# Performance work log

Measured on AMD Instinct MI355X. Metric: run time of the kernel, lower is better.

## Reference

```python
import jax, jax.numpy as jnp
import numpy as np
from jax import lax

TAU = 0.25
N_TIMESTEPS = 12
OUTPUT_TICKS = 4
INPUT_DIM = 1024
HIDDEN = 1024
OUTPUT_DIM = 1024
CLEANUP = 512
BATCH = 1024
W_SD = 0.1


def setup_inputs() -> dict:
    key = jax.random.key(0)
    ks = jax.random.split(key, 6)
    inputs = jax.random.normal(ks[0], (BATCH, N_TIMESTEPS, INPUT_DIM), dtype=jnp.float32)
    w_oh = W_SD * jax.random.normal(ks[1], (INPUT_DIM, HIDDEN), dtype=jnp.float32)
    w_hp = W_SD * jax.random.normal(ks[2], (HIDDEN, OUTPUT_DIM), dtype=jnp.float32)
    w_pp = W_SD * jax.random.normal(ks[3], (OUTPUT_DIM, OUTPUT_DIM), dtype=jnp.float32)
    w_pc = W_SD * jax.random.normal(ks[4], (OUTPUT_DIM, CLEANUP), dtype=jnp.float32)
    w_cp = W_SD * jax.random.normal(ks[5], (CLEANUP, OUTPUT_DIM), dtype=jnp.float32)
    bias_h = jnp.zeros((HIDDEN,), jnp.float32)
    bias_p = jnp.zeros((OUTPUT_DIM,), jnp.float32)
    bias_c = jnp.zeros((CLEANUP,), jnp.float32)
    return {"inputs": inputs, "w_oh": w_oh, "w_hp": w_hp, "w_pp": w_pp,
            "w_pc": w_pc, "w_cp": w_cp, "bias_h": bias_h, "bias_p": bias_p,
            "bias_c": bias_c}


def reference(inputs, w_oh, w_hp, w_pp, w_pc, w_cp, bias_h, bias_p, bias_c):
    B = inputs.shape[0]
    act = jax.nn.sigmoid
    # time-major input stream: step t consumes o_input[:, t-1, :]
    x = jnp.swapaxes(inputs, 0, 1)  # [T, B, I]

    in_h0 = jnp.zeros((B, HIDDEN), jnp.float32)
    in_p0 = jnp.zeros((B, OUTPUT_DIM), jnp.float32)
    in_c0 = jnp.zeros((B, CLEANUP), jnp.float32)
    carry0 = (in_h0, in_p0, in_c0, in_h0 + 0.5, in_p0 + 0.5, in_c0 + 0.5)

    def step(carry, o_t):
        in_h, in_p, in_c, a_h, a_p, a_c = carry
        # leaky-integrator blends; hp/pp/cp/pc all use PREVIOUS step activations
        h = TAU * (o_t @ w_oh + bias_h) + (1.0 - TAU) * in_h
        p = TAU * (a_h @ w_hp + a_p @ w_pp + a_c @ w_cp + bias_p) + (1.0 - TAU) * in_p
        c = TAU * (a_p @ w_pc + bias_c) + (1.0 - TAU) * in_c
        a_p_new = act(p)
        new_carry = (h, p, c, act(h), a_p_new, act(c))
        return new_carry, a_p_new

    _, act_p_seq = lax.scan(step, carry0, x)  # [T, B, OUTPUT_DIM]
    return act_p_seq[-OUTPUT_TICKS:]  # [OUTPUT_TICKS, B, OUTPUT_DIM]
```

## Files before the change

kernel.cpp:

```cpp
#include <hip/hip_runtime.h>
#include <cstdint>
#include <cstddef>


typedef _Float16 half8 __attribute__((ext_vector_type(8)));
typedef float floatx4 __attribute__((ext_vector_type(4)));

__device__ __forceinline__ void async_cp16(const void* g, void* l) {
  __builtin_amdgcn_global_load_lds(
      (const __attribute__((address_space(1))) void*)g,
      (__attribute__((address_space(3))) void*)l, 16, 0, 0);
}

__device__ __forceinline__ float sigmoidf_(float x) {
  return 1.f / (1.f + __expf(-x));
}

__global__ __launch_bounds__(256) void k_transpose(
    const float* __restrict__ src, int K, int N,
    _Float16* __restrict__ dst, int dst_ld, int k_off) {
  __shared__ float tile[64][65];
  const int k0 = blockIdx.y * 64, n0 = blockIdx.x * 64;
  const int tx = threadIdx.x & 63, ty = threadIdx.x >> 6;
#pragma unroll
  for (int j = 0; j < 16; ++j) {
    int kr = j * 4 + ty;
    tile[kr][tx] = src[(size_t)(k0 + kr) * N + n0 + tx];
  }
  __syncthreads();
#pragma unroll
  for (int j = 0; j < 16; ++j) {
    int nr = j * 4 + ty;
    dst[(size_t)(n0 + nr) * dst_ld + k_off + k0 + tx] = (_Float16)tile[tx][nr];
  }
}

__global__ __launch_bounds__(256) void k_pack_frag(
    const float* __restrict__ src, int N, _Float16* __restrict__ dst,
    int kStride, int kOffChunks) {
  __shared__ float tile[64][65];
  const int k0 = blockIdx.y * 64, n0 = blockIdx.x * 64;
  const int tx = threadIdx.x & 63, ty = threadIdx.x >> 6;
#pragma unroll
  for (int jj = 0; jj < 16; ++jj) {
    int kr = jj * 4 + ty;
    tile[kr][tx] = src[(size_t)(k0 + kr) * N + n0 + tx];
  }
  __syncthreads();
  const int j = threadIdx.x >> 6, lane = threadIdx.x & 63;
  const int r16 = lane & 15, quad = lane >> 4;
#pragma unroll
  for (int c = 0; c < 2; ++c) {
    half8 v;
#pragma unroll
    for (int u = 0; u < 8; ++u)
      v[u] = (_Float16)tile[c * 32 + quad * 8 + u][j * 16 + r16];
    const int kcG = kOffChunks + blockIdx.y * 2 + c;
    *(half8*)(dst + ((size_t)(blockIdx.x * kStride + kcG) * 4 + j) * 512 +
              lane * 8) = v;
  }
}

__global__ __launch_bounds__(256) void k_prep(
    const float* __restrict__ x, _Float16* __restrict__ U,
    _Float16* __restrict__ AH0, _Float16* __restrict__ AP0,
    _Float16* __restrict__ AC0, float* __restrict__ Pst,
    float* __restrict__ Cst) {
  const int id = blockIdx.x * 256 + threadIdx.x;
  const int b = id >> 10, i = id & 1023;
  const float* xb = x + (size_t)b * 12 * 1024 + i;
  float g = 0.f;
#pragma unroll
  for (int t = 0; t < 11; ++t) {
    g = xb[t * 1024] + 0.75f * g;
    U[(size_t)t * 1048576 + id] = (_Float16)g;
  }
  AH0[id] = (_Float16)0.5f;
  AP0[id] = (_Float16)0.5f;
  Pst[id] = 0.f;
  if (i < 512) {
    AC0[b * 512 + i] = (_Float16)0.5f;
    Cst[b * 512 + i] = 0.f;
  }
}

__global__ __launch_bounds__(256, 3) void k_gemm_big(
    const _Float16* __restrict__ A, const _Float16* __restrict__ B,
    const float* __restrict__ bias, _Float16* __restrict__ dst, int mode) {
  __shared__ __align__(16) _Float16 sA[128 * 64];
  __shared__ __align__(16) _Float16 sB[128 * 64];
  const int tid = threadIdx.x;
  const int lane = tid & 63, w = tid >> 6;
  const int lin = blockIdx.x;
  const int chunk = gridDim.x >> 6;
  const int xcd = lin & 7;
  const int j0 = lin >> 3;
  const int bx = j0 & 7;
  const int by = xcd * chunk + (j0 >> 3);
  const int mBase = by * 128, nBase = bx * 128;
  const int r16 = lane & 15, quad = lane >> 4;
  const int lrow = lane >> 3;
  const int gsw = ((lane & 7) ^ lrow) * 8;
  const int wr = w >> 1, wc = w & 1;

  const floatx4 zero = {0.f, 0.f, 0.f, 0.f};
  floatx4 acc[4][4];
#pragma unroll
  for (int i = 0; i < 4; ++i)
#pragma unroll
    for (int j = 0; j < 4; ++j) acc[i][j] = zero;

  const _Float16* Abase = A + (size_t)(mBase + w * 32 + lrow) * 1024 + gsw;
  const _Float16* Bbase = B + (size_t)(nBase + w * 32 + lrow) * 1024 + gsw;
  _Float16* sAw = sA + (w * 32) * 64;
  _Float16* sBw = sB + (w * 32) * 64;
  const _Float16* sa = sA + (size_t)wr * 64 * 64;
  const _Float16* sb = sB + (size_t)wc * 64 * 64;

  for (int kt = 0; kt < 16; ++kt) {
    const int k0 = kt << 6;
#pragma unroll
    for (int q = 0; q < 4; ++q)
      async_cp16(Abase + (size_t)q * 8192 + k0, sAw + q * 512);
#pragma unroll
    for (int q = 0; q < 4; ++q)
      async_cp16(Bbase + (size_t)q * 8192 + k0, sBw + q * 512);
    asm volatile("s_waitcnt vmcnt(0)" ::: "memory");
    __syncthreads();
#pragma unroll
    for (int kk = 0; kk < 2; ++kk) {
      const int sw = ((kk * 4 + quad) ^ (r16 & 7)) * 8;
      half8 af[4], bf[4];
#pragma unroll
      for (int i = 0; i < 4; ++i)
        af[i] = *(const half8*)&sa[(i * 16 + r16) * 64 + sw];
#pragma unroll
      for (int j = 0; j < 4; ++j)
        bf[j] = *(const half8*)&sb[(j * 16 + r16) * 64 + sw];
#pragma unroll
      for (int i = 0; i < 4; ++i)
#pragma unroll
        for (int j = 0; j < 4; ++j)
          acc[i][j] = __builtin_amdgcn_mfma_f32_16x16x32_f16(af[i], bf[j],
                                                             acc[i][j], 0, 0, 0);
    }
    __syncthreads();
  }

  if (mode == 0) {
    const int tm1 = mBase >> 10;
    const float beta = 1.f - __powf(0.75f, (float)(tm1 + 1));
    _Float16* o = dst + (size_t)(mBase + 1024) * 1024;
#pragma unroll
    for (int i = 0; i < 4; ++i)
#pragma unroll
      for (int j = 0; j < 4; ++j) {
        const int n = nBase + wc * 64 + j * 16 + r16;
#pragma unroll
        for (int r = 0; r < 4; ++r) {
          const int row = wr * 64 + i * 16 + quad * 4 + r;
          const float h = 0.25f * acc[i][j][r] + beta * bias[n];
          o[(size_t)row * 1024 + n] = (_Float16)sigmoidf_(h);
        }
      }
  } else {
    _Float16* o = dst + (size_t)mBase * 1024;
#pragma unroll
    for (int i = 0; i < 4; ++i)
#pragma unroll
      for (int j = 0; j < 4; ++j) {
        const int n = nBase + wc * 64 + j * 16 + r16;
#pragma unroll
        for (int r = 0; r < 4; ++r) {
          const int row = wr * 64 + i * 16 + quad * 4 + r;
          o[(size_t)row * 1024 + n] = (_Float16)(0.25f * (acc[i][j][r] + bias[n]));
        }
      }
  }
}

__global__ __launch_bounds__(256, 3) void k_step(
    const _Float16* __restrict__ Qt, const _Float16* __restrict__ APc,
    const _Float16* __restrict__ ACc, _Float16* __restrict__ APn,
    _Float16* __restrict__ ACn, const _Float16* __restrict__ Wrf,
    const _Float16* __restrict__ Wcf, const float* __restrict__ bias_c,
    float* __restrict__ Pst, float* __restrict__ Cst,
    float* __restrict__ out_t) {
  __shared__ float red[4][2][4][4][64];
  const int lane = threadIdx.x & 63, w = threadIdx.x >> 6;
  const int r16 = lane & 15, quad = lane >> 4;
  const int blk = blockIdx.x;
  const bool isP = blk < 512;
  int mBase, nt;
  if (isP) {
    mBase = (blk >> 4) * 32;
    nt = blk & 15;
  } else {
    const int b = blk - 512;
    mBase = (b >> 3) * 32;
    nt = b & 7;
  }
  const int nBase = nt * 64;
  const floatx4 zero = {0.f, 0.f, 0.f, 0.f};
  floatx4 acc[2][4];
#pragma unroll
  for (int i = 0; i < 2; ++i)
#pragma unroll
    for (int j = 0; j < 4; ++j) acc[i][j] = zero;

  half8 abuf[4][2], bbuf[4][4];
  auto MM = [&](half8* af, half8* bf) {
#pragma unroll
    for (int i = 0; i < 2; ++i)
#pragma unroll
      for (int j = 0; j < 4; ++j)
        acc[i][j] = __builtin_amdgcn_mfma_f32_16x16x32_f16(af[i], bf[j],
                                                           acc[i][j], 0, 0, 0);
  };

  if (isP) {
    const int kcBase = w * 12;
    auto LDA = [&](int c) {
      const int kc = kcBase + c, kg = kc * 32;
      half8* af = abuf[c & 3];
      if (kc < 32) {
        af[0] = *(const half8*)(APc + (size_t)(mBase + r16) * 1024 + kg + quad * 8);
        af[1] = *(const half8*)(APc + (size_t)(mBase + 16 + r16) * 1024 + kg + quad * 8);
      } else {
        af[0] = *(const half8*)(ACc + (size_t)(mBase + r16) * 512 + (kg - 1024) + quad * 8);
        af[1] = *(const half8*)(ACc + (size_t)(mBase + 16 + r16) * 512 + (kg - 1024) + quad * 8);
      }
    };
    auto LDB = [&](int c) {
      const int kc = kcBase + c;
      const _Float16* wp = Wrf + (size_t)(nt * 48 + kc) * 2048 + lane * 8;
      half8* bf = bbuf[c & 3];
#pragma unroll
      for (int j = 0; j < 4; ++j) bf[j] = *(const half8*)(wp + j * 512);
    };
    LDA(0); LDA(1); LDA(2); LDA(3);
    LDB(0); LDB(1); LDB(2);
#pragma unroll
    for (int c = 0; c < 12; ++c) {
      if (c + 3 < 12) LDB(c + 3);
      MM(abuf[c & 3], bbuf[c & 3]);
      if (c + 4 < 12) LDA(c + 4);
    }
  } else {
    const int kcBase = w * 8;
    auto LDA = [&](int c) {
      const int kc = kcBase + c, kg = kc * 32;
      half8* af = abuf[c & 3];
      af[0] = *(const half8*)(APc + (size_t)(mBase + r16) * 1024 + kg + quad * 8);
      af[1] = *(const half8*)(APc + (size_t)(mBase + 16 + r16) * 1024 + kg + quad * 8);
    };
    auto LDB = [&](int c) {
      const int kc = kcBase + c;
      const _Float16* wp = Wcf + (size_t)(nt * 32 + kc) * 2048 + lane * 8;
      half8* bf = bbuf[c & 3];
#pragma unroll
      for (int j = 0; j < 4; ++j) bf[j] = *(const half8*)(wp + j * 512);
    };
    LDA(0); LDA(1); LDA(2); LDA(3);
    LDB(0); LDB(1); LDB(2);
#pragma unroll
    for (int c = 0; c < 8; ++c) {
      if (c + 3 < 8) LDB(c + 3);
      MM(abuf[c & 3], bbuf[c & 3]);
      if (c + 4 < 8) LDA(c + 4);
    }
  }

  const int n_ep = nBase + w * 16 + r16;
  _Float16 qv[2][4];
  float sv[2][4];
  float biasn = 0.f;
  if (isP) {
#pragma unroll
    for (int i = 0; i < 2; ++i)
#pragma unroll
      for (int r = 0; r < 4; ++r) {
        const size_t o = (size_t)(mBase + i * 16 + quad * 4 + r) * 1024 + n_ep;
        qv[i][r] = Qt[o];
        sv[i][r] = Pst[o];
      }
  } else {
    biasn = bias_c[n_ep];
#pragma unroll
    for (int i = 0; i < 2; ++i)
#pragma unroll
      for (int r = 0; r < 4; ++r) {
        const size_t o = (size_t)(mBase + i * 16 + quad * 4 + r) * 512 + n_ep;
        sv[i][r] = Cst[o];
      }
  }

#pragma unroll
  for (int i = 0; i < 2; ++i)
#pragma unroll
    for (int j = 0; j < 4; ++j)
#pragma unroll
      for (int r = 0; r < 4; ++r) red[w][i][j][r][lane] = acc[i][j][r];
  asm volatile("s_waitcnt lgkmcnt(0)" ::: "memory");
  __builtin_amdgcn_s_barrier();

  if (isP) {
#pragma unroll
    for (int i = 0; i < 2; ++i) {
#pragma unroll
      for (int r = 0; r < 4; ++r) {
        float v = 0.f;
#pragma unroll
        for (int q = 0; q < 4; ++q) v += red[q][i][w][r][lane];
        const int b = mBase + i * 16 + quad * 4 + r;
        const size_t o = (size_t)b * 1024 + n_ep;
        const float pn = 0.25f * v + (float)qv[i][r] + 0.75f * sv[i][r];
        Pst[o] = pn;
        const float a = sigmoidf_(pn);
        APn[o] = (_Float16)a;
        if (out_t) out_t[o] = a;
      }
    }
  } else {
#pragma unroll
    for (int i = 0; i < 2; ++i) {
#pragma unroll
      for (int r = 0; r < 4; ++r) {
        float v = 0.f;
#pragma unroll
        for (int q = 0; q < 4; ++q) v += red[q][i][w][r][lane];
        const int b = mBase + i * 16 + quad * 4 + r;
        const size_t o = (size_t)b * 512 + n_ep;
        const float cn = 0.25f * (v + biasn) + 0.75f * sv[i][r];
        Cst[o] = cn;
        ACn[o] = (_Float16)sigmoidf_(cn);
      }
    }
  }
}

extern "C" void kernel_launch(void* const* d_in, const int* in_sizes, int n_in,
                              void* d_out, int out_size, void* d_ws,
                              size_t ws_size, hipStream_t stream) {
  const float* x      = (const float*)d_in[0];
  const float* w_oh   = (const float*)d_in[1];
  const float* w_hp   = (const float*)d_in[2];
  const float* w_pp   = (const float*)d_in[3];
  const float* w_pc   = (const float*)d_in[4];
  const float* w_cp   = (const float*)d_in[5];
  const float* bias_h = (const float*)d_in[6];
  const float* bias_p = (const float*)d_in[7];
  const float* bias_c = (const float*)d_in[8];
  float* out = (float*)d_out;

  uint8_t* p = (uint8_t*)d_ws;
  _Float16* Wrf  = (_Float16*)p; p += (size_t)1024 * 1536 * 2;
  _Float16* Wcf  = (_Float16*)p; p += (size_t)512 * 1024 * 2;
  _Float16* WohT = (_Float16*)p; p += (size_t)1024 * 1024 * 2;
  _Float16* Whp  = (_Float16*)p; p += (size_t)1024 * 1024 * 2;
  _Float16* U    = (_Float16*)p; p += (size_t)11 * 1048576 * 2;
  _Float16* AH   = (_Float16*)p; p += (size_t)12 * 1048576 * 2;
  _Float16* Q    = (_Float16*)p; p += (size_t)12 * 1048576 * 2;
  _Float16* AP0  = (_Float16*)p; p += (size_t)1048576 * 2;
  _Float16* AP1  = (_Float16*)p; p += (size_t)1048576 * 2;
  _Float16* AC0  = (_Float16*)p; p += (size_t)512 * 1024 * 2;
  _Float16* AC1  = (_Float16*)p; p += (size_t)512 * 1024 * 2;
  float* Pst = (float*)p; p += (size_t)1048576 * 4;
  float* Cst = (float*)p; p += (size_t)512 * 1024 * 4;

  const dim3 blk256(256);
  k_transpose<<<dim3(16, 16), blk256, 0, stream>>>(w_oh, 1024, 1024, WohT, 1024, 0);
  k_transpose<<<dim3(16, 16), blk256, 0, stream>>>(w_hp, 1024, 1024, Whp, 1024, 0);
  k_pack_frag<<<dim3(16, 16), blk256, 0, stream>>>(w_pp, 1024, Wrf, 48, 0);
  k_pack_frag<<<dim3(16, 8),  blk256, 0, stream>>>(w_cp, 1024, Wrf, 48, 32);
  k_pack_frag<<<dim3(8, 16),  blk256, 0, stream>>>(w_pc, 512, Wcf, 32, 0);
  k_prep<<<4096, blk256, 0, stream>>>(x, U, AH, AP0, AC0, Pst, Cst);
  k_gemm_big<<<dim3(8 * 88), blk256, 0, stream>>>(U, WohT, bias_h, AH, 0);
  k_gemm_big<<<dim3(8 * 96), blk256, 0, stream>>>(AH, Whp, bias_p, Q, 1);
  for (int t = 0; t < 12; ++t) {
    const _Float16* APc = (t & 1) ? AP1 : AP0;
    _Float16* APn       = (t & 1) ? AP0 : AP1;
    const _Float16* ACc = (t & 1) ? AC1 : AC0;
    _Float16* ACn       = (t & 1) ? AC0 : AC1;
    float* ot = (t >= 8) ? out + (size_t)(t - 8) * 1048576 : (float*)nullptr;
    k_step<<<dim3(768), blk256, 0, stream>>>(Q + (size_t)t * 1048576, APc,
                                             ACc, APn, ACn, Wrf, Wcf, bias_c,
                                             Pst, Cst, ot);
  }
}
```

Before: 385.2 us.

## Halve step-kernel N tile to double block count and merge weight-prep kernels

The recurrent step kernel now gives each block a 32x32 output tile instead of 32x64. This doubles the grid to 1536 blocks and raises the occupancy hint from 3 to 6 blocks per CU, with fewer accumulators and a shallower 3-stage load pipeline. The five weight transpose/pack kernels are merged into one launch to cut launch overhead. In exchange, activation rows are re-read by twice as many blocks and there is less prefetch depth per block.

```diff
diff --git a/kernel.cpp b/kernel.cpp
--- a/kernel.cpp
+++ b/kernel.cpp
@@ -16,11 +16,10 @@
   return 1.f / (1.f + __expf(-x));
 }
 
-__global__ __launch_bounds__(256) void k_transpose(
-    const float* __restrict__ src, int K, int N,
-    _Float16* __restrict__ dst, int dst_ld, int k_off) {
-  __shared__ float tile[64][65];
-  const int k0 = blockIdx.y * 64, n0 = blockIdx.x * 64;
+__device__ __forceinline__ void transpose_dev(
+    const float* __restrict__ src, int N, _Float16* __restrict__ dst,
+    int dst_ld, int k_off, int bx, int by, float (*tile)[65]) {
+  const int k0 = by * 64, n0 = bx * 64;
   const int tx = threadIdx.x & 63, ty = threadIdx.x >> 6;
 #pragma unroll
   for (int j = 0; j < 16; ++j) {
@@ -35,11 +34,10 @@
   }
 }
 
-__global__ __launch_bounds__(256) void k_pack_frag(
+__device__ __forceinline__ void pack_dev(
     const float* __restrict__ src, int N, _Float16* __restrict__ dst,
-    int kStride, int kOffChunks) {
-  __shared__ float tile[64][65];
-  const int k0 = blockIdx.y * 64, n0 = blockIdx.x * 64;
+    int kStride, int kOffChunks, int bx, int by, float (*tile)[65]) {
+  const int k0 = by * 64, n0 = bx * 64;
   const int tx = threadIdx.x & 63, ty = threadIdx.x >> 6;
 #pragma unroll
   for (int jj = 0; jj < 16; ++jj) {
@@ -55,9 +53,33 @@
 #pragma unroll
     for (int u = 0; u < 8; ++u)
       v[u] = (_Float16)tile[c * 32 + quad * 8 + u][j * 16 + r16];
-    const int kcG = kOffChunks + blockIdx.y * 2 + c;
-    *(half8*)(dst + ((size_t)(blockIdx.x * kStride + kcG) * 4 + j) * 512 +
-              lane * 8) = v;
+    const int kcG = kOffChunks + by * 2 + c;
+    *(half8*)(dst + ((size_t)(bx * kStride + kcG) * 4 + j) * 512 + lane * 8) = v;
+  }
+}
+
+__global__ __launch_bounds__(256) void k_wprep(
+    const float* __restrict__ w_oh, const float* __restrict__ w_hp,
+    const float* __restrict__ w_pp, const float* __restrict__ w_cp,
+    const float* __restrict__ w_pc, _Float16* __restrict__ WohT,
+    _Float16* __restrict__ Whp, _Float16* __restrict__ Wrf,
+    _Float16* __restrict__ Wcf) {
+  __shared__ float tile[64][65];
+  const int blk = blockIdx.x;
+  if (blk < 256) {
+    transpose_dev(w_oh, 1024, WohT, 1024, 0, blk & 15, blk >> 4, tile);
+  } else if (blk < 512) {
+    const int t = blk - 256;
+    transpose_dev(w_hp, 1024, Whp, 1024, 0, t & 15, t >> 4, tile);
+  } else if (blk < 768) {
+    const int t = blk - 512;
+    pack_dev(w_pp, 1024, Wrf, 48, 0, t & 15, t >> 4, tile);
+  } else if (blk < 896) {
+    const int t = blk - 768;
+    pack_dev(w_cp, 1024, Wrf, 48, 32, t & 15, t >> 4, tile);
+  } else {
+    const int t = blk - 896;
+    pack_dev(w_pc, 512, Wcf, 32, 0, t & 7, t >> 3, tile);
   }
 }
 
@@ -179,41 +201,42 @@
   }
 }
 
-__global__ __launch_bounds__(256, 3) void k_step(
+__global__ __launch_bounds__(256, 6) void k_step(
     const _Float16* __restrict__ Qt, const _Float16* __restrict__ APc,
     const _Float16* __restrict__ ACc, _Float16* __restrict__ APn,
     _Float16* __restrict__ ACn, const _Float16* __restrict__ Wrf,
     const _Float16* __restrict__ Wcf, const float* __restrict__ bias_c,
     float* __restrict__ Pst, float* __restrict__ Cst,
     float* __restrict__ out_t) {
-  __shared__ float red[4][2][4][4][64];
+  __shared__ float red[4][2][2][4][64];
   const int lane = threadIdx.x & 63, w = threadIdx.x >> 6;
   const int r16 = lane & 15, quad = lane >> 4;
   const int blk = blockIdx.x;
-  const bool isP = blk < 512;
-  int mBase, nt;
+  const bool isP = blk < 1024;
+  int mBase, nBase, ntG, jhalf;
   if (isP) {
-    mBase = (blk >> 4) * 32;
-    nt = blk & 15;
-  } else {
-    const int b = blk - 512;
-    mBase = (b >> 3) * 32;
-    nt = b & 7;
-  }
-  const int nBase = nt * 64;
+    mBase = (blk >> 5) * 32;
+    const int nt = blk & 31;
+    nBase = nt * 32; ntG = nt >> 1; jhalf = nt & 1;
+  } else {
+    const int b = blk - 1024;
+    mBase = (b >> 4) * 32;
+    const int nt = b & 15;
+    nBase = nt * 32; ntG = nt >> 1; jhalf = nt & 1;
+  }
   const floatx4 zero = {0.f, 0.f, 0.f, 0.f};
-  floatx4 acc[2][4];
+  floatx4 acc[2][2];
 #pragma unroll
   for (int i = 0; i < 2; ++i)
 #pragma unroll
-    for (int j = 0; j < 4; ++j) acc[i][j] = zero;
-
-  half8 abuf[4][2], bbuf[4][4];
+    for (int j = 0; j < 2; ++j) acc[i][j] = zero;
+
+  half8 abuf[3][2], bbuf[3][2];
   auto MM = [&](half8* af, half8* bf) {
 #pragma unroll
     for (int i = 0; i < 2; ++i)
 #pragma unroll
-      for (int j = 0; j < 4; ++j)
+      for (int j = 0; j < 2; ++j)
         acc[i][j] = __builtin_amdgcn_mfma_f32_16x16x32_f16(af[i], bf[j],
                                                            acc[i][j], 0, 0, 0);
   };
@@ -222,7 +245,7 @@
     const int kcBase = w * 12;
     auto LDA = [&](int c) {
       const int kc = kcBase + c, kg = kc * 32;
-      half8* af = abuf[c & 3];
+      half8* af = abuf[c % 3];
       if (kc < 32) {
         af[0] = *(const half8*)(APc + (size_t)(mBase + r16) * 1024 + kg + quad * 8);
         af[1] = *(const half8*)(APc + (size_t)(mBase + 16 + r16) * 1024 + kg + quad * 8);
@@ -233,72 +256,69 @@
     };
     auto LDB = [&](int c) {
       const int kc = kcBase + c;
-      const _Float16* wp = Wrf + (size_t)(nt * 48 + kc) * 2048 + lane * 8;
-      half8* bf = bbuf[c & 3];
-#pragma unroll
-      for (int j = 0; j < 4; ++j) bf[j] = *(const half8*)(wp + j * 512);
+      const _Float16* wp =
+          Wrf + ((size_t)(ntG * 48 + kc) * 4 + jhalf * 2) * 512 + lane * 8;
+      half8* bf = bbuf[c % 3];
+      bf[0] = *(const half8*)(wp);
+      bf[1] = *(const half8*)(wp + 512);
     };
-    LDA(0); LDA(1); LDA(2); LDA(3);
+    LDA(0); LDA(1); LDA(2);
     LDB(0); LDB(1); LDB(2);
 #pragma unroll
     for (int c = 0; c < 12; ++c) {
-      if (c + 3 < 12) LDB(c + 3);
-      MM(abuf[c & 3], bbuf[c & 3]);
-      if (c + 4 < 12) LDA(c + 4);
+      MM(abuf[c % 3], bbuf[c % 3]);
+      if (c + 3 < 12) { LDB(c + 3); LDA(c + 3); }
     }
   } else {
     const int kcBase = w * 8;
     auto LDA = [&](int c) {
       const int kc = kcBase + c, kg = kc * 32;
-      half8* af = abuf[c & 3];
+      half8* af = abuf[c % 3];
       af[0] = *(const half8*)(APc + (size_t)(mBase + r16) * 1024 + kg + quad * 8);
       af[1] = *(const half8*)(APc + (size_t)(mBase + 16 + r16) * 1024 + kg + quad * 8);
     };
     auto LDB = [&](int c) {
       const int kc = kcBase + c;
-      const _Float16* wp = Wcf + (size_t)(nt * 32 + kc) * 2048 + lane * 8;
-      half8* bf = bbuf[c & 3];
-#pragma unroll
-      for (int j = 0; j < 4; ++j) bf[j] = *(const half8*)(wp + j * 512);
+      const _Float16* wp =
+          Wcf + ((size_t)(ntG * 32 + kc) * 4 + jhalf * 2) * 512 + lane * 8;
+      half8* bf = bbuf[c % 3];
+      bf[0] = *(const half8*)(wp);
+      bf[1] = *(const half8*)(wp + 512);
     };
-    LDA(0); LDA(1); LDA(2); LDA(3);
+    LDA(0); LDA(1); LDA(2);
     LDB(0); LDB(1); LDB(2);
 #pragma unroll
     for (int c = 0; c < 8; ++c) {
-      if (c + 3 < 8) LDB(c + 3);
-      MM(abuf[c & 3], bbuf[c & 3]);
-      if (c + 4 < 8) LDA(c + 4);
-    }
-  }
-
-  const int n_ep = nBase + w * 16 + r16;
-  _Float16 qv[2][4];
-  float sv[2][4];
+      MM(abuf[c % 3], bbuf[c % 3]);
+      if (c + 3 < 8) { LDB(c + 3); LDA(c + 3); }
+    }
+  }
+
+  const int i_ep = w >> 1, j_ep = w & 1;
+  const int n_ep = nBase + j_ep * 16 + r16;
+  _Float16 qv[4];
+  float sv[4];
   float biasn = 0.f;
   if (isP) {
 #pragma unroll
-    for (int i = 0; i < 2; ++i)
-#pragma unroll
-      for (int r = 0; r < 4; ++r) {
-        const size_t o = (size_t)(mBase + i * 16 + quad * 4 + r) * 1024 + n_ep;
-        qv[i][r] = Qt[o];
-        sv[i][r] = Pst[o];
-      }
+    for (int r = 0; r < 4; ++r) {
+      const size_t o = (size_t)(mBase + i_ep * 16 + quad * 4 + r) * 1024 + n_ep;
+      qv[r] = Qt[o];
+      sv[r] = Pst[o];
+    }
   } else {
     biasn = bias_c[n_ep];
 #pragma unroll
-    for (int i = 0; i < 2; ++i)
-#pragma unroll
-      for (int r = 0; r < 4; ++r) {
-        const size_t o = (size_t)(mBase + i * 16 + quad * 4 + r) * 512 + n_ep;
-        sv[i][r] = Cst[o];
-      }
+    for (int r = 0; r < 4; ++r) {
+      const size_t o = (size_t)(mBase + i_ep * 16 + quad * 4 + r) * 512 + n_ep;
+      sv[r] = Cst[o];
+    }
   }
 
 #pragma unroll
   for (int i = 0; i < 2; ++i)
 #pragma unroll
-    for (int j = 0; j < 4; ++j)
+    for (int j = 0; j < 2; ++j)
 #pragma unroll
       for (int r = 0; r < 4; ++r) red[w][i][j][r][lane] = acc[i][j][r];
   asm volatile("s_waitcnt lgkmcnt(0)" ::: "memory");
@@ -306,35 +326,29 @@
 
   if (isP) {
 #pragma unroll
-    for (int i = 0; i < 2; ++i) {
-#pragma unroll
-      for (int r = 0; r < 4; ++r) {
-        float v = 0.f;
-#pragma unroll
-        for (int q = 0; q < 4; ++q) v += red[q][i][w][r][lane];
-        const int b = mBase + i * 16 + quad * 4 + r;
-        const size_t o = (size_t)b * 1024 + n_ep;
-        const float pn = 0.25f * v + (float)qv[i][r] + 0.75f * sv[i][r];
-        Pst[o] = pn;
-        const float a = sigmoidf_(pn);
-        APn[o] = (_Float16)a;
-        if (out_t) out_t[o] = a;
-      }
-    }
-  } else {
-#pragma unroll
-    for (int i = 0; i < 2; ++i) {
-#pragma unroll
-      for (int r = 0; r < 4; ++r) {
-        float v = 0.f;
-#pragma unroll
-        for (int q = 0; q < 4; ++q) v += red[q][i][w][r][lane];
-        const int b = mBase + i * 16 + quad * 4 + r;
-        const size_t o = (size_t)b * 512 + n_ep;
-        const float cn = 0.25f * (v + biasn) + 0.75f * sv[i][r];
-        Cst[o] = cn;
-        ACn[o] = (_Float16)sigmoidf_(cn);
-      }
+    for (int r = 0; r < 4; ++r) {
+      float v = 0.f;
+#pragma unroll
+      for (int q = 0; q < 4; ++q) v += red[q][i_ep][j_ep][r][lane];
+      const int b = mBase + i_ep * 16 + quad * 4 + r;
+      const size_t o = (size_t)b * 1024 + n_ep;
+      const float pn = 0.25f * v + (float)qv[r] + 0.75f * sv[r];
+      Pst[o] = pn;
+      const float a = sigmoidf_(pn);
+      APn[o] = (_Float16)a;
+      if (out_t) out_t[o] = a;
+    }
+  } else {
+#pragma unroll
+    for (int r = 0; r < 4; ++r) {
+      float v = 0.f;
+#pragma unroll
+      for (int q = 0; q < 4; ++q) v += red[q][i_ep][j_ep][r][lane];
+      const int b = mBase + i_ep * 16 + quad * 4 + r;
+      const size_t o = (size_t)b * 512 + n_ep;
+      const float cn = 0.25f * (v + biasn) + 0.75f * sv[r];
+      Cst[o] = cn;
+      ACn[o] = (_Float16)sigmoidf_(cn);
     }
   }
 }
@@ -369,11 +383,8 @@
   float* Cst = (float*)p; p += (size_t)512 * 1024 * 4;
 
   const dim3 blk256(256);
-  k_transpose<<<dim3(16, 16), blk256, 0, stream>>>(w_oh, 1024, 1024, WohT, 1024, 0);
-  k_transpose<<<dim3(16, 16), blk256, 0, stream>>>(w_hp, 1024, 1024, Whp, 1024, 0);
-  k_pack_frag<<<dim3(16, 16), blk256, 0, stream>>>(w_pp, 1024, Wrf, 48, 0);
-  k_pack_frag<<<dim3(16, 8),  blk256, 0, stream>>>(w_cp, 1024, Wrf, 48, 32);
-  k_pack_frag<<<dim3(8, 16),  blk256, 0, stream>>>(w_pc, 512, Wcf, 32, 0);
+  k_wprep<<<dim3(1024), blk256, 0, stream>>>(w_oh, w_hp, w_pp, w_cp, w_pc,
+                                             WohT, Whp, Wrf, Wcf);
   k_prep<<<4096, blk256, 0, stream>>>(x, U, AH, AP0, AC0, Pst, Cst);
   k_gemm_big<<<dim3(8 * 88), blk256, 0, stream>>>(U, WohT, bias_h, AH, 0);
   k_gemm_big<<<dim3(8 * 96), blk256, 0, stream>>>(AH, Whp, bias_p, Q, 1);
@@ -383,8 +394,8 @@
     const _Float16* ACc = (t & 1) ? AC1 : AC0;
     _Float16* ACn       = (t & 1) ? AC0 : AC1;
     float* ot = (t >= 8) ? out + (size_t)(t - 8) * 1048576 : (float*)nullptr;
-    k_step<<<dim3(768), blk256, 0, stream>>>(Q + (size_t)t * 1048576, APc,
-                                             ACc, APn, ACn, Wrf, Wcf, bias_c,
-                                             Pst, Cst, ot);
-  }
-}
+    k_step<<<dim3(1536), blk256, 0, stream>>>(Q + (size_t)t * 1048576, APc,
+                                              ACc, APn, ACn, Wrf, Wcf, bias_c,
+                                              Pst, Cst, ot);
+  }
+}
```

New measurement: 491.2 us. +27.5%, slower.

## Merge weight-prep kernels and shrink big GEMM N-tile to 64 for occupancy

Applied to the files above, without the earlier changes.

Folds the five weight transpose/pack launches into a single k_wprep kernel that dispatches on block index, removing four launches. It also halves the N tile of the big GEMMs from 128 to 64, doubling the grid and raising the launch-bounds occupancy hint from 3 to 5. The smaller tile gives more blocks to spread across CUs, but each A tile is now fetched for twice as many blocks and there is less MFMA work per LDS load.

```diff
diff --git a/kernel.cpp b/kernel.cpp
--- a/kernel.cpp
+++ b/kernel.cpp
@@ -16,11 +16,10 @@
   return 1.f / (1.f + __expf(-x));
 }
 
-__global__ __launch_bounds__(256) void k_transpose(
-    const float* __restrict__ src, int K, int N,
-    _Float16* __restrict__ dst, int dst_ld, int k_off) {
-  __shared__ float tile[64][65];
-  const int k0 = blockIdx.y * 64, n0 = blockIdx.x * 64;
+__device__ __forceinline__ void transpose_dev(
+    const float* __restrict__ src, int N, _Float16* __restrict__ dst,
+    int dst_ld, int k_off, int bx, int by, float (*tile)[65]) {
+  const int k0 = by * 64, n0 = bx * 64;
   const int tx = threadIdx.x & 63, ty = threadIdx.x >> 6;
 #pragma unroll
   for (int j = 0; j < 16; ++j) {
@@ -35,11 +34,10 @@
   }
 }
 
-__global__ __launch_bounds__(256) void k_pack_frag(
+__device__ __forceinline__ void pack_dev(
     const float* __restrict__ src, int N, _Float16* __restrict__ dst,
-    int kStride, int kOffChunks) {
-  __shared__ float tile[64][65];
-  const int k0 = blockIdx.y * 64, n0 = blockIdx.x * 64;
+    int kStride, int kOffChunks, int bx, int by, float (*tile)[65]) {
+  const int k0 = by * 64, n0 = bx * 64;
   const int tx = threadIdx.x & 63, ty = threadIdx.x >> 6;
 #pragma unroll
   for (int jj = 0; jj < 16; ++jj) {
@@ -55,9 +53,33 @@
 #pragma unroll
     for (int u = 0; u < 8; ++u)
       v[u] = (_Float16)tile[c * 32 + quad * 8 + u][j * 16 + r16];
-    const int kcG = kOffChunks + blockIdx.y * 2 + c;
-    *(half8*)(dst + ((size_t)(blockIdx.x * kStride + kcG) * 4 + j) * 512 +
-              lane * 8) = v;
+    const int kcG = kOffChunks + by * 2 + c;
+    *(half8*)(dst + ((size_t)(bx * kStride + kcG) * 4 + j) * 512 + lane * 8) = v;
+  }
+}
+
+__global__ __launch_bounds__(256) void k_wprep(
+    const float* __restrict__ w_oh, const float* __restrict__ w_hp,
+    const float* __restrict__ w_pp, const float* __restrict__ w_cp,
+    const float* __restrict__ w_pc, _Float16* __restrict__ WohT,
+    _Float16* __restrict__ Whp, _Float16* __restrict__ Wrf,
+    _Float16* __restrict__ Wcf) {
+  __shared__ float tile[64][65];
+  const int blk = blockIdx.x;
+  if (blk < 256) {
+    transpose_dev(w_oh, 1024, WohT, 1024, 0, blk & 15, blk >> 4, tile);
+  } else if (blk < 512) {
+    const int t = blk - 256;
+    transpose_dev(w_hp, 1024, Whp, 1024, 0, t & 15, t >> 4, tile);
+  } else if (blk < 768) {
+    const int t = blk - 512;
+    pack_dev(w_pp, 1024, Wrf, 48, 0, t & 15, t >> 4, tile);
+  } else if (blk < 896) {
+    const int t = blk - 768;
+    pack_dev(w_cp, 1024, Wrf, 48, 32, t & 15, t >> 4, tile);
+  } else {
+    const int t = blk - 896;
+    pack_dev(w_pc, 512, Wcf, 32, 0, t & 7, t >> 3, tile);
   }
 }
 
@@ -84,38 +106,38 @@
   }
 }
 
-__global__ __launch_bounds__(256, 3) void k_gemm_big(
+__global__ __launch_bounds__(256, 5) void k_gemm_big(
     const _Float16* __restrict__ A, const _Float16* __restrict__ B,
     const float* __restrict__ bias, _Float16* __restrict__ dst, int mode) {
   __shared__ __align__(16) _Float16 sA[128 * 64];
-  __shared__ __align__(16) _Float16 sB[128 * 64];
+  __shared__ __align__(16) _Float16 sB[64 * 64];
   const int tid = threadIdx.x;
   const int lane = tid & 63, w = tid >> 6;
   const int lin = blockIdx.x;
-  const int chunk = gridDim.x >> 6;
+  const int chunk = gridDim.x >> 7;
   const int xcd = lin & 7;
   const int j0 = lin >> 3;
-  const int bx = j0 & 7;
-  const int by = xcd * chunk + (j0 >> 3);
-  const int mBase = by * 128, nBase = bx * 128;
+  const int bx = j0 & 15;
+  const int by = xcd * chunk + (j0 >> 4);
+  const int mBase = by * 128, nBase = bx * 64;
   const int r16 = lane & 15, quad = lane >> 4;
   const int lrow = lane >> 3;
   const int gsw = ((lane & 7) ^ lrow) * 8;
   const int wr = w >> 1, wc = w & 1;
 
   const floatx4 zero = {0.f, 0.f, 0.f, 0.f};
-  floatx4 acc[4][4];
+  floatx4 acc[4][2];
 #pragma unroll
   for (int i = 0; i < 4; ++i)
 #pragma unroll
-    for (int j = 0; j < 4; ++j) acc[i][j] = zero;
+    for (int j = 0; j < 2; ++j) acc[i][j] = zero;
 
   const _Float16* Abase = A + (size_t)(mBase + w * 32 + lrow) * 1024 + gsw;
-  const _Float16* Bbase = B + (size_t)(nBase + w * 32 + lrow) * 1024 + gsw;
+  const _Float16* Bbase = B + (size_t)(nBase + w * 16 + lrow) * 1024 + gsw;
   _Float16* sAw = sA + (w * 32) * 64;
-  _Float16* sBw = sB + (w * 32) * 64;
+  _Float16* sBw = sB + (w * 16) * 64;
   const _Float16* sa = sA + (size_t)wr * 64 * 64;
-  const _Float16* sb = sB + (size_t)wc * 64 * 64;
+  const _Float16* sb = sB + (size_t)wc * 32 * 64;
 
   for (int kt = 0; kt < 16; ++kt) {
     const int k0 = kt << 6;
@@ -123,24 +145,24 @@
     for (int q = 0; q < 4; ++q)
       async_cp16(Abase + (size_t)q * 8192 + k0, sAw + q * 512);
 #pragma unroll
-    for (int q = 0; q < 4; ++q)
+    for (int q = 0; q < 2; ++q)
       async_cp16(Bbase + (size_t)q * 8192 + k0, sBw + q * 512);
     asm volatile("s_waitcnt vmcnt(0)" ::: "memory");
     __syncthreads();
 #pragma unroll
     for (int kk = 0; kk < 2; ++kk) {
       const int sw = ((kk * 4 + quad) ^ (r16 & 7)) * 8;
-      half8 af[4], bf[4];
+      half8 af[4], bf[2];
 #pragma unroll
       for (int i = 0; i < 4; ++i)
         af[i] = *(const half8*)&sa[(i * 16 + r16) * 64 + sw];
 #pragma unroll
-      for (int j = 0; j < 4; ++j)
+      for (int j = 0; j < 2; ++j)
         bf[j] = *(const half8*)&sb[(j * 16 + r16) * 64 + sw];
 #pragma unroll
       for (int i = 0; i < 4; ++i)
 #pragma unroll
-        for (int j = 0; j < 4; ++j)
+        for (int j = 0; j < 2; ++j)
           acc[i][j] = __builtin_amdgcn_mfma_f32_16x16x32_f16(af[i], bf[j],
                                                              acc[i][j], 0, 0, 0);
     }
@@ -154,8 +176,8 @@
 #pragma unroll
     for (int i = 0; i < 4; ++i)
 #pragma unroll
-      for (int j = 0; j < 4; ++j) {
-        const int n = nBase + wc * 64 + j * 16 + r16;
+      for (int j = 0; j < 2; ++j) {
+        const int n = nBase + wc * 32 + j * 16 + r16;
 #pragma unroll
         for (int r = 0; r < 4; ++r) {
           const int row = wr * 64 + i * 16 + quad * 4 + r;
@@ -168,8 +190,8 @@
 #pragma unroll
     for (int i = 0; i < 4; ++i)
 #pragma unroll
-      for (int j = 0; j < 4; ++j) {
-        const int n = nBase + wc * 64 + j * 16 + r16;
+      for (int j = 0; j < 2; ++j) {
+        const int n = nBase + wc * 32 + j * 16 + r16;
 #pragma unroll
         for (int r = 0; r < 4; ++r) {
           const int row = wr * 64 + i * 16 + quad * 4 + r;
@@ -369,14 +391,11 @@
   float* Cst = (float*)p; p += (size_t)512 * 1024 * 4;
 
   const dim3 blk256(256);
-  k_transpose<<<dim3(16, 16), blk256, 0, stream>>>(w_oh, 1024, 1024, WohT, 1024, 0);
-  k_transpose<<<dim3(16, 16), blk256, 0, stream>>>(w_hp, 1024, 1024, Whp, 1024, 0);
-  k_pack_frag<<<dim3(16, 16), blk256, 0, stream>>>(w_pp, 1024, Wrf, 48, 0);
-  k_pack_frag<<<dim3(16, 8),  blk256, 0, stream>>>(w_cp, 1024, Wrf, 48, 32);
-  k_pack_frag<<<dim3(8, 16),  blk256, 0, stream>>>(w_pc, 512, Wcf, 32, 0);
+  k_wprep<<<dim3(1024), blk256, 0, stream>>>(w_oh, w_hp, w_pp, w_cp, w_pc,
+                                             WohT, Whp, Wrf, Wcf);
   k_prep<<<4096, blk256, 0, stream>>>(x, U, AH, AP0, AC0, Pst, Cst);
-  k_gemm_big<<<dim3(8 * 88), blk256, 0, stream>>>(U, WohT, bias_h, AH, 0);
-  k_gemm_big<<<dim3(8 * 96), blk256, 0, stream>>>(AH, Whp, bias_p, Q, 1);
+  k_gemm_big<<<dim3(16 * 88), blk256, 0, stream>>>(U, WohT, bias_h, AH, 0);
+  k_gemm_big<<<dim3(16 * 96), blk256, 0, stream>>>(AH, Whp, bias_p, Q, 1);
   for (int t = 0; t < 12; ++t) {
     const _Float16* APc = (t & 1) ? AP1 : AP0;
     _Float16* APn       = (t & 1) ? AP0 : AP1;
```

After: 391.0 us. Within noise of the previous version (+1.5%).
